# Kernel optimization log

Hardware: AMD Instinct MI355X
Metric: run time of the kernel (lower is better)

The kernel has to match this reference:

```python
import jax, jax.numpy as jnp
import numpy as np

D = 128
POI = 8192
N_HE = 51      # hyperedges (users) in HG_pu
N_UC = 42      # user/category slots at front of UI embedding
LAYERS = 2
TEMP = 0.2


def _l2norm(x):
    n = jnp.linalg.norm(x, axis=-1, keepdims=True)
    return x / jnp.maximum(n, 1e-12)


def _cheby_linear(x, coeffs):
    # x: [N, in], coeffs: [in, out, order+1] -> [N, out]
    x = jnp.tanh(x)
    order = coeffs.shape[-1] - 1
    Ts = [jnp.ones_like(x), x]
    for _ in range(order - 1):
        Ts.append(2.0 * x * Ts[-1] - Ts[-2])
    T = jnp.stack(Ts, axis=-1)  # [N, in, order+1]
    return jnp.einsum('nik,iok->no', T, coeffs)


def _gated_kan(x1, x2, cr, ci):
    # FFT-gated fusion of two [N, D] embeddings (GatedKAN1)
    X1 = jnp.fft.fft(x1, axis=-1)
    X2 = jnp.fft.fft(x2, axis=-1)
    gr = jax.nn.sigmoid(_cheby_linear(X1.real, cr) + _cheby_linear(X2.real, cr))
    fr = gr * X1.real + (1.0 - gr) * X2.real
    gi = jax.nn.sigmoid(_cheby_linear(X1.imag, ci) + _cheby_linear(X2.imag, ci))
    fi = gi * X1.imag + (1.0 - gi) * X2.imag
    return jnp.fft.ifft(fr + 1j * fi, axis=-1).real.astype(x1.dtype)


def _info_nce(z1, z2, temp=TEMP):
    # symmetric InfoNCE with arange labels (diagonal positives)
    z1 = _l2norm(z1)
    z2 = _l2norm(z2)
    sim = jnp.matmul(z1, z2.T) / temp
    l1 = -jnp.mean(jnp.diagonal(jax.nn.log_softmax(sim, axis=1)))
    l2 = -jnp.mean(jnp.diagonal(jax.nn.log_softmax(sim.T, axis=1)))
    return 0.5 * (l1 + l2)


def _hconv(e, HG_pu, HG_up, layers):
    # mean over layer outputs of hypergraph propagation HG_up @ (HG_pu @ e)
    acc = e
    for _ in range(layers):
        e = jnp.matmul(HG_up, jnp.matmul(HG_pu, e))
        acc = acc + e
    return acc / (layers + 1)


def _gconv(e, A, layers):
    acc = e
    for _ in range(layers):
        e = jnp.matmul(A, e)
        acc = acc + e
    return acc / (layers + 1)


def setup_inputs() -> dict:
    key = jax.random.key(0)
    ks = jax.random.split(key, 13)
    inp = {
        'poi_w': jax.random.normal(ks[0], (POI + 1, D), jnp.float32) * 0.02,
        'ui_w': jax.random.normal(ks[1], (POI + 1 + N_UC, D), jnp.float32) * 0.02,
        'w_gate_col': jax.random.normal(ks[2], (D, D), jnp.float32) * 0.08,
        'b_gate_col': jax.random.normal(ks[3], (1, D), jnp.float32) * 0.08,
        'w_gate_U': jax.random.normal(ks[4], (D, D), jnp.float32) * 0.08,
        'b_gate_U': jax.random.normal(ks[5], (1, D), jnp.float32) * 0.08,
        'cheb_real': jax.random.normal(ks[6], (D, D, 4), jnp.float32) / (D * 4),
        'cheb_imag': jax.random.normal(ks[7], (D, D, 4), jnp.float32) / (D * 4),
        'HG_pu': jax.random.uniform(ks[8], (N_HE, POI), jnp.float32) / POI,
        'HG_up': jax.random.uniform(ks[9], (POI, N_HE), jnp.float32) / N_HE,
        'U_I': jax.random.uniform(ks[10], (POI + N_UC, POI + N_UC), jnp.float32) / (POI + N_UC),
        'noise1': jax.random.normal(ks[11], (POI, D), jnp.float32) * 0.1,
        'noise2': jax.random.normal(ks[12], (POI + N_UC, D), jnp.float32) * 0.1,
        'target': 100,
        'user_col': 7,
        'user_ui': 5,
    }
    return inp


def reference(poi_w, ui_w, w_gate_col, b_gate_col, w_gate_U, b_gate_U,
              cheb_real, cheb_imag, HG_pu, HG_up, U_I, noise1, noise2,
              target, user_col, user_ui):
    # gated embedding transforms
    pw = poi_w[:-1]
    col_gate = pw * jax.nn.sigmoid(jnp.matmul(pw, w_gate_col) + b_gate_col)   # [POI, D]
    uw = ui_w[:-1]
    U_gate = uw * jax.nn.sigmoid(jnp.matmul(uw, w_gate_U) + b_gate_U)          # [POI+42, D]

    # hypergraph view
    hg = _l2norm(_hconv(col_gate, HG_pu, HG_up, LAYERS))                        # [POI, D]
    level_loss = _info_nce(hg, hg + noise1)
    hg_users = jnp.matmul(HG_pu, hg)                                            # [51, D]
    hg_user = hg_users[user_col]
    user_cl = hg_users[9:]                                                      # [42, D]

    # user-item graph view
    ue = _l2norm(_gconv(U_gate, U_I, LAYERS))                                   # [POI+42, D]
    level_loss1 = _info_nce(ue, ue + noise2)
    poi_e = ue[N_UC:]                                                           # [POI, D]
    users_emb = ue[user_ui]
    user_c = ue[:N_UC]                                                          # [42, D]

    # FFT-gated Chebyshev-KAN fusion
    final_p = _gated_kan(hg, poi_e, cheb_real, cheb_imag)                       # [POI, D]
    final_u = users_emb + hg_user                                               # [D]
    output = jnp.matmul(final_p, final_u)                                       # [POI]

    pred_loss = -jax.nn.log_softmax(output)[target]
    ssl_p = _info_nce(hg, poi_e)
    ssl = _info_nce(user_c, user_cl)
    loss = pred_loss + (level_loss1 + level_loss) + (ssl_p + ssl)
    return (loss, output)
```

## Files before the change

kernel.cpp:

```cpp
#include <hip/hip_runtime.h>
#include <math.h>

#define D 128
#define P 8192
#define PU 8234
#define NHE 51
#define NUC 42
#define KP 8256

typedef __attribute__((ext_vector_type(8))) short short8v;
typedef __attribute__((ext_vector_type(8))) unsigned short ushort8v;
typedef __attribute__((ext_vector_type(4))) float f32x4;

__device__ inline void atomAddF(float* p, float v) {
#if defined(__HIP_PLATFORM_AMD__)
    unsafeAtomicAdd(p, v);
#else
    atomicAdd(p, v);
#endif
}

__device__ inline unsigned short bfr(float f) {
    unsigned int u = __float_as_uint(f);
    u += 0x7fffu + ((u >> 16) & 1u);
    return (unsigned short)(u >> 16);
}

__global__ void k_tables(float* Cm, float* Sm) {
    int idx = blockIdx.x * 256 + threadIdx.x;
    if (idx >= D * D) return;
    int k = idx >> 7, t = idx & 127;
    int m = (k * t) & 127;
    float ang = (float)m * 0.049087385212340517f;
    Cm[idx] = cosf(ang);
    Sm[idx] = -sinf(ang);
}

__global__ void k_reshape(const float* __restrict__ cr, const float* __restrict__ ci,
                          float* __restrict__ Wr, float* __restrict__ Wi) {
    int idx = blockIdx.x * 256 + threadIdx.x;
    if (idx >= 512 * D) return;
    int o = idx & 127;
    int ik = idx >> 7;
    int i = ik >> 2, kk = ik & 3;
    Wr[idx] = cr[(i * 128 + o) * 4 + kk];
    Wi[idx] = ci[(i * 128 + o) * 4 + kk];
}

#define GEMM_BODY(K_)                                                     \
    {                                                                     \
        float a[4], b[8];                                                 \
        _Pragma("unroll") for (int r = 0; r < 4; r++) a[r] = As[ty + 16 * r][K_]; \
        _Pragma("unroll") for (int c = 0; c < 8; c++) b[c] = Bs[K_][tx + 16 * c]; \
        _Pragma("unroll") for (int r = 0; r < 4; r++)                     \
            _Pragma("unroll") for (int c = 0; c < 8; c++)                 \
                acc[r][c] += a[r] * b[c];                                 \
    }

__global__ __launch_bounds__(256) void k_gemm(const float* __restrict__ A, int lda,
                                              const float* __restrict__ B,
                                              float* __restrict__ C,
                                              int M, int K, float alpha, int klen) {
    __shared__ float As[64][33];
    __shared__ float Bs[32][128];
    const int t = threadIdx.x;
    const int tx = t & 15, ty = t >> 4;
    const int i0 = blockIdx.x * 64;
    const int kbeg = blockIdx.y * klen;
    const int kend = min(K, kbeg + klen);
    float acc[4][8];
#pragma unroll
    for (int r = 0; r < 4; r++)
#pragma unroll
        for (int c = 0; c < 8; c++) acc[r][c] = 0.f;

    for (int k0 = kbeg; k0 < kend; k0 += 32) {
#pragma unroll
        for (int q = 0; q < 2; q++) {
            int idx = t + q * 256;
            int row = idx >> 3;
            int col = (idx & 7) * 4;
            int gi = i0 + row;
#pragma unroll
            for (int u = 0; u < 4; u++) {
                int gk = k0 + col + u;
                As[row][col + u] = (gi < M && gk < kend) ? A[(size_t)gi * lda + gk] : 0.f;
            }
        }
#pragma unroll
        for (int q = 0; q < 4; q++) {
            int idx = t + q * 256;
            int row = idx >> 5;
            int col4 = (idx & 31) * 4;
            int gk = k0 + row;
            float4 v = make_float4(0.f, 0.f, 0.f, 0.f);
            if (gk < kend) v = *reinterpret_cast<const float4*>(B + (size_t)gk * 128 + col4);
            *reinterpret_cast<float4*>(&Bs[row][col4]) = v;
        }
        __syncthreads();
        int klim = min(32, kend - k0);
        if (klim == 32) {
#pragma unroll
            for (int k = 0; k < 32; k++) GEMM_BODY(k)
        } else {
            for (int k = 0; k < klim; k++) GEMM_BODY(k)
        }
        __syncthreads();
    }
#pragma unroll
    for (int r = 0; r < 4; r++) {
        int gi = i0 + ty + 16 * r;
        if (gi < M) {
#pragma unroll
            for (int c = 0; c < 8; c++)
                atomAddF(&C[(size_t)gi * 128 + tx + 16 * c], alpha * acc[r][c]);
        }
    }
}

__global__ void k_small_pu(const float* __restrict__ PUm, const float* __restrict__ X,
                           float* __restrict__ T, int Kn) {
    int i = blockIdx.x;
    int klen = (Kn + gridDim.y - 1) / gridDim.y;
    int kbeg = blockIdx.y * klen;
    int kend = min(Kn, kbeg + klen);
    int t = threadIdx.x;
    int d = t & 127, half = t >> 7;
    float acc = 0.f;
    for (int k = kbeg + half; k < kend; k += 2)
        acc += PUm[(size_t)i * Kn + k] * X[(size_t)k * 128 + d];
    atomAddF(&T[i * 128 + d], acc);
}

__global__ void k_gate_ep(const float* __restrict__ X, const float* __restrict__ pre,
                          const float* __restrict__ bias, float* __restrict__ out, int n) {
    int idx = blockIdx.x * 256 + threadIdx.x;
    if (idx < n) {
        float s = pre[idx] + bias[idx & 127];
        s = 1.f / (1.f + expf(-s));
        out[idx] = X[idx] * s;
    }
}

__global__ void k_acc3norm(const float* __restrict__ a, const float* __restrict__ b,
                           const float* __restrict__ c, float* __restrict__ out) {
    __shared__ float red[128];
    size_t i = blockIdx.x;
    int d = threadIdx.x;
    float v = (a[i * 128 + d] + b[i * 128 + d] + c[i * 128 + d]) * (1.f / 3.f);
    red[d] = v * v;
    __syncthreads();
    for (int s = 64; s > 0; s >>= 1) {
        if (d < s) red[d] += red[d + s];
        __syncthreads();
    }
    float inv = 1.f / fmaxf(sqrtf(red[0]), 1e-12f);
    out[i * 128 + d] = v * inv;
}

__global__ void k_prep(const float* __restrict__ X, const float* __restrict__ Yadd,
                       float scale, unsigned short* __restrict__ Zb) {
    __shared__ float red[128];
    size_t i = blockIdx.x;
    int d = threadIdx.x;
    float v = X[i * 128 + d];
    if (Yadd) v += Yadd[i * 128 + d];
    red[d] = v * v;
    __syncthreads();
    for (int s = 64; s > 0; s >>= 1) {
        if (d < s) red[d] += red[d + s];
        __syncthreads();
    }
    float inv = scale / fmaxf(sqrtf(red[0]), 1e-12f);
    Zb[i * 128 + d] = bfr(v * inv);
}

__global__ __launch_bounds__(256) void k_rowcol_mfma(
    const unsigned short* __restrict__ Za, int n1,
    const unsigned short* __restrict__ Zb, int n2,
    float* __restrict__ rowsum, float* __restrict__ colsum, float* __restrict__ diagsum) {
    __shared__ ushort8v As[2048];
    __shared__ ushort8v Bs[2048];
    const int t = threadIdx.x;
    const int i0 = blockIdx.x * 128, j0 = blockIdx.y * 128;
#pragma unroll
    for (int u = 0; u < 8; ++u) {
        int g = t + u * 256;
        int row = g >> 4, c = g & 15;
        int sw = (row << 4) | (c ^ (row & 15));
        ushort8v va = (ushort8v){0, 0, 0, 0, 0, 0, 0, 0};
        ushort8v vb = va;
        if (i0 + row < n1) va = *(const ushort8v*)(Za + ((size_t)(i0 + row) << 7) + c * 8);
        if (j0 + row < n2) vb = *(const ushort8v*)(Zb + ((size_t)(j0 + row) << 7) + c * 8);
        As[sw] = va;
        Bs[sw] = vb;
    }
    __syncthreads();
    const int l = t & 63, w = t >> 6;
    const int wy = w >> 1, wx = w & 1;
    const int lr = l & 15, lg = l >> 4;
    f32x4 acc[4][4];
#pragma unroll
    for (int mi = 0; mi < 4; ++mi)
#pragma unroll
        for (int ni = 0; ni < 4; ++ni) acc[mi][ni] = (f32x4){0.f, 0.f, 0.f, 0.f};

#pragma unroll
    for (int ks = 0; ks < 4; ++ks) {
        short8v a[4], b[4];
        int c = ks * 4 + lg;
#pragma unroll
        for (int mi = 0; mi < 4; ++mi) {
            int r = wy * 64 + mi * 16 + lr;
            a[mi] = __builtin_bit_cast(short8v, As[(r << 4) | (c ^ (r & 15))]);
            int r2 = wx * 64 + mi * 16 + lr;
            b[mi] = __builtin_bit_cast(short8v, Bs[(r2 << 4) | (c ^ (r2 & 15))]);
        }
#pragma unroll
        for (int mi = 0; mi < 4; ++mi)
#pragma unroll
            for (int ni = 0; ni < 4; ++ni)
                acc[mi][ni] = __builtin_amdgcn_mfma_f32_16x16x32_bf16(a[mi], b[ni], acc[mi][ni], 0, 0, 0);
    }
    float colp[4] = {0.f, 0.f, 0.f, 0.f};
    float dsum = 0.f;
#pragma unroll
    for (int mi = 0; mi < 4; ++mi) {
#pragma unroll
        for (int rg = 0; rg < 4; ++rg) {
            int grow = i0 + wy * 64 + mi * 16 + lg * 4 + rg;
            float rowp = 0.f;
#pragma unroll
            for (int ni = 0; ni < 4; ++ni) {
                int gcol = j0 + wx * 64 + ni * 16 + lr;
                float v = acc[mi][ni][rg];
                bool ok = (grow < n1) && (gcol < n2);
                float e = ok ? __expf(v) : 0.f;
                rowp += e;
                colp[ni] += e;
                if (ok && grow == gcol) dsum += v;
            }
            rowp += __shfl_xor(rowp, 1);
            rowp += __shfl_xor(rowp, 2);
            rowp += __shfl_xor(rowp, 4);
            rowp += __shfl_xor(rowp, 8);
            if (lr == 0 && grow < n1) atomAddF(&rowsum[grow], rowp);
        }
    }
#pragma unroll
    for (int ni = 0; ni < 4; ++ni) {
        float cp = colp[ni];
        cp += __shfl_xor(cp, 16);
        cp += __shfl_xor(cp, 32);
        int gcol = j0 + wx * 64 + ni * 16 + lr;
        if (lg == 0 && gcol < n2) atomAddF(&colsum[gcol], cp);
    }
    if (blockIdx.x == blockIdx.y) {
        dsum += __shfl_xor(dsum, 1);
        dsum += __shfl_xor(dsum, 2);
        dsum += __shfl_xor(dsum, 4);
        dsum += __shfl_xor(dsum, 8);
        dsum += __shfl_xor(dsum, 16);
        dsum += __shfl_xor(dsum, 32);
        if (l == 0) atomAddF(diagsum, dsum);
    }
}

__global__ __launch_bounds__(256) void k_tconv(const float* __restrict__ B,
                                               unsigned short* __restrict__ Bt, int K) {
    __shared__ float tile[32][33];
    int tx = threadIdx.x & 31, ty = threadIdx.x >> 5;
    int k0 = blockIdx.x * 32, c0 = blockIdx.y * 32;
#pragma unroll
    for (int q = 0; q < 4; ++q) {
        int k = k0 + ty + q * 8;
        tile[ty + q * 8][tx] = (k < K) ? B[(size_t)k * 128 + c0 + tx] : 0.f;
    }
    __syncthreads();
#pragma unroll
    for (int q = 0; q < 4; ++q) {
        int c = c0 + ty + q * 8;
        Bt[(size_t)c * KP + k0 + tx] = bfr(tile[tx][ty + q * 8]);
    }
}

__global__ __launch_bounds__(256) void k_gconv(const float* __restrict__ A,
                                               const unsigned short* __restrict__ Bt,
                                               float* __restrict__ C,
                                               int M, int K, int klen) {
    const int t = threadIdx.x;
    const int l = t & 63, w = t >> 6;
    const int lr = l & 15, lg = l >> 4;
    const int r0 = blockIdx.x * 128 + w * 32;
    const int kbeg = blockIdx.y * klen;
    const int kend = min(K, kbeg + klen);
    f32x4 acc[2][8];
#pragma unroll
    for (int mi = 0; mi < 2; ++mi)
#pragma unroll
        for (int ni = 0; ni < 8; ++ni) acc[mi][ni] = (f32x4){0.f, 0.f, 0.f, 0.f};
    size_t rA[2];
    rA[0] = (size_t)min(r0 + lr, M - 1) * (size_t)K;
    rA[1] = (size_t)min(r0 + 16 + lr, M - 1) * (size_t)K;

    for (int k0 = kbeg; k0 < kend; k0 += 32) {
        int kf = k0 + lg * 8;
        short8v a[2];
        if (kf + 8 <= K) {
#pragma unroll
            for (int mi = 0; mi < 2; ++mi) {
                const float* p = A + rA[mi] + kf;
                float2 f0 = *(const float2*)(p);
                float2 f1 = *(const float2*)(p + 2);
                float2 f2 = *(const float2*)(p + 4);
                float2 f3 = *(const float2*)(p + 6);
                short8v v;
                v[0] = (short)bfr(f0.x); v[1] = (short)bfr(f0.y);
                v[2] = (short)bfr(f1.x); v[3] = (short)bfr(f1.y);
                v[4] = (short)bfr(f2.x); v[5] = (short)bfr(f2.y);
                v[6] = (short)bfr(f3.x); v[7] = (short)bfr(f3.y);
                a[mi] = v;
            }
        } else {
#pragma unroll
            for (int mi = 0; mi < 2; ++mi) {
                short8v v;
#pragma unroll
                for (int j = 0; j < 8; ++j) {
                    int kk = kf + j;
                    v[j] = (kk < K) ? (short)bfr(A[rA[mi] + kk]) : (short)0;
                }
                a[mi] = v;
            }
        }
        short8v b[8];
#pragma unroll
        for (int ni = 0; ni < 8; ++ni)
            b[ni] = *(const short8v*)(Bt + (size_t)(ni * 16 + lr) * KP + kf);
#pragma unroll
        for (int mi = 0; mi < 2; ++mi)
#pragma unroll
            for (int ni = 0; ni < 8; ++ni)
                acc[mi][ni] = __builtin_amdgcn_mfma_f32_16x16x32_bf16(a[mi], b[ni], acc[mi][ni], 0, 0, 0);
    }
#pragma unroll
    for (int mi = 0; mi < 2; ++mi) {
#pragma unroll
        for (int rg = 0; rg < 4; ++rg) {
            int gr = r0 + mi * 16 + lg * 4 + rg;
            if (gr < M) {
#pragma unroll
                for (int ni = 0; ni < 8; ++ni)
                    atomAddF(&C[(size_t)gr * 128 + ni * 16 + lr], acc[mi][ni][rg]);
            }
        }
    }
}

__global__ void k_nce_reduce(const float* __restrict__ rs, const float* __restrict__ cs,
                             const float* __restrict__ diag, int n, float* __restrict__ loss) {
    __shared__ float red[256];
    int t = threadIdx.x;
    float s = 0.f;
    for (int i = blockIdx.x * 256 + t; i < n; i += gridDim.x * 256)
        s += logf(rs[i]) + logf(cs[i]);
    red[t] = s;
    __syncthreads();
    for (int st = 128; st > 0; st >>= 1) {
        if (t < st) red[t] += red[t + st];
        __syncthreads();
    }
    if (t == 0) {
        float v = 0.5f * red[0] / (float)n;
        if (blockIdx.x == 0) v -= diag[0] / (float)n;
        atomAddF(loss, v);
    }
}

__global__ void k_ssl(const float* __restrict__ UE, const float* __restrict__ HGU,
                      float* __restrict__ loss) {
    __shared__ float A[NUC][128], B[NUC][128];
    __shared__ float sim[NUC][NUC];
    __shared__ float invA[NUC], invB[NUC];
    __shared__ float pr[64];
    int t = threadIdx.x;
    for (int idx = t; idx < NUC * 128; idx += 256) {
        A[idx >> 7][idx & 127] = UE[idx];
        B[idx >> 7][idx & 127] = HGU[9 * 128 + idx];
    }
    __syncthreads();
    if (t < 2 * NUC) {
        int i = (t < NUC) ? t : t - NUC;
        float s = 0.f;
        if (t < NUC) {
            for (int d = 0; d < 128; d++) { float v = A[i][d]; s += v * v; }
            invA[i] = 1.f / fmaxf(sqrtf(s), 1e-12f);
        } else {
            for (int d = 0; d < 128; d++) { float v = B[i][d]; s += v * v; }
            invB[i] = 1.f / fmaxf(sqrtf(s), 1e-12f);
        }
    }
    __syncthreads();
    for (int idx = t; idx < NUC * NUC; idx += 256) {
        int i = idx / NUC, j = idx % NUC;
        float s = 0.f;
        for (int d = 0; d < 128; d++) s += A[i][d] * B[j][d];
        sim[i][j] = s * invA[i] * invB[j] * 5.0f;
    }
    __syncthreads();
    float part = 0.f;
    if (t < NUC) {
        float rsu = 0.f, csu = 0.f;
        for (int j = 0; j < NUC; j++) {
            rsu += __expf(sim[t][j]);
            csu += __expf(sim[j][t]);
        }
        part = 0.5f * (logf(rsu) + logf(csu)) - sim[t][t];
    }
    if (t < 64) pr[t] = (t < NUC) ? part : 0.f;
    __syncthreads();
    if (t == 0) {
        float s = 0.f;
        for (int i = 0; i < NUC; i++) s += pr[i];
        atomAddF(loss, s / (float)NUC);
    }
}

__global__ void k_features(const float* __restrict__ Xa, const float* __restrict__ Xb,
                           float* __restrict__ G, int n) {
    int idx = blockIdx.x * 256 + threadIdx.x;
    if (idx < n) {
        float x1 = tanhf(Xa[idx]), x2 = tanhf(Xb[idx]);
        float4 w;
        w.x = 2.0f;
        w.y = x1 + x2;
        w.z = (2.f * x1 * x1 - 1.f) + (2.f * x2 * x2 - 1.f);
        w.w = x1 * (4.f * x1 * x1 - 3.f) + x2 * (4.f * x2 * x2 - 3.f);
        *reinterpret_cast<float4*>(G + (size_t)idx * 4) = w;
    }
}

__global__ void k_mix(const float* __restrict__ pre, float* __restrict__ a,
                      const float* __restrict__ b, int n) {
    int idx = blockIdx.x * 256 + threadIdx.x;
    if (idx < n) {
        float g = 1.f / (1.f + expf(-pre[idx]));
        a[idx] = g * a[idx] + (1.f - g) * b[idx];
    }
}

__global__ void k_finalu(const float* __restrict__ UE, const float* __restrict__ HGU,
                         const int* __restrict__ uui, const int* __restrict__ ucol,
                         float* __restrict__ fu) {
    int d = threadIdx.x;
    fu[d] = UE[(size_t)(*uui) * 128 + d] + HGU[(*ucol) * 128 + d];
}

__global__ void k_outvec(const float* __restrict__ FP, const float* __restrict__ fu,
                         float* __restrict__ out) {
    __shared__ float red[128];
    size_t i = blockIdx.x;
    int d = threadIdx.x;
    red[d] = FP[i * 128 + d] * fu[d];
    __syncthreads();
    for (int s = 64; s > 0; s >>= 1) {
        if (d < s) red[d] += red[d + s];
        __syncthreads();
    }
    if (d == 0) out[i] = red[0];
}

__global__ void k_predloss(const float* __restrict__ ov, const int* __restrict__ tgt,
                           float* __restrict__ loss) {
    __shared__ float red[256];
    int t = threadIdx.x;
    float m = -1e30f;
    for (int i = t; i < P; i += 256) m = fmaxf(m, ov[i]);
    red[t] = m;
    __syncthreads();
    for (int s = 128; s > 0; s >>= 1) {
        if (t < s) red[t] = fmaxf(red[t], red[t + s]);
        __syncthreads();
    }
    float mg = red[0];
    __syncthreads();
    float ssum = 0.f;
    for (int i = t; i < P; i += 256) ssum += __expf(ov[i] - mg);
    red[t] = ssum;
    __syncthreads();
    for (int s = 128; s > 0; s >>= 1) {
        if (t < s) red[t] += red[t + s];
        __syncthreads();
    }
    if (t == 0) {
        float lse = mg + logf(red[0]);
        atomAddF(loss, lse - ov[*tgt]);
    }
}

__global__ void k_writeloss(const float* __restrict__ sc, float* __restrict__ out) {
    out[0] = sc[0];
}

extern "C" void kernel_launch(void* const* d_in, const int* in_sizes, int n_in,
                              void* d_out, int out_size, void* d_ws, size_t ws_size,
                              hipStream_t stream) {
    const float* poi_w  = (const float*)d_in[0];
    const float* ui_w   = (const float*)d_in[1];
    const float* Wc     = (const float*)d_in[2];
    const float* bc     = (const float*)d_in[3];
    const float* WU     = (const float*)d_in[4];
    const float* bU     = (const float*)d_in[5];
    const float* cr     = (const float*)d_in[6];
    const float* ci     = (const float*)d_in[7];
    const float* HGpu   = (const float*)d_in[8];
    const float* HGup   = (const float*)d_in[9];
    const float* UI     = (const float*)d_in[10];
    const float* noise1 = (const float*)d_in[11];
    const float* noise2 = (const float*)d_in[12];
    const int* target   = (const int*)d_in[13];
    const int* ucol     = (const int*)d_in[14];
    const int* uui      = (const int*)d_in[15];
    float* out = (float*)d_out;

    float* ws = (float*)d_ws;
    size_t o = 0;
    auto alloc = [&](size_t n) { float* p = ws + o; o += n; return p; };
    float* H   = alloc((size_t)P * D);
    float* UE  = alloc((size_t)PU * D);
    float* B1  = alloc((size_t)PU * D);
    float* B2  = alloc((size_t)PU * D);
    float* B3  = alloc((size_t)PU * D);
    float* B4  = alloc((size_t)PU * D);
    float* G   = alloc((size_t)P * 512);
    float* PRE = alloc((size_t)P * D);
    float* TS  = alloc(NHE * D);
    float* HGU = alloc(NHE * D);
    float* CM  = alloc(D * D);
    float* SM  = alloc(D * D);
    float* WR  = alloc(512 * D);
    float* WI  = alloc(512 * D);
    float* RS  = alloc(8240);
    float* CS  = alloc(8240);
    float* SC  = alloc(16);
    float* FU  = alloc(D);
    unsigned short* ZA = (unsigned short*)alloc((size_t)PU * D / 2);
    unsigned short* ZB = (unsigned short*)alloc((size_t)PU * D / 2);
    unsigned short* ZC = (unsigned short*)alloc((size_t)PU * D / 2);
    unsigned short* BT = (unsigned short*)alloc((size_t)D * KP / 2);
    if (o * sizeof(float) > ws_size) return;

    auto Z = [&](float* p, size_t n) { hipMemsetAsync(p, 0, n * sizeof(float), stream); };
    auto GEMM = [&](const float* A, int lda, const float* B, float* C, int M, int K,
                    int ysplit, float alpha) {
        int klen = (K + ysplit - 1) / ysplit;
        dim3 g((M + 63) / 64, ysplit);
        k_gemm<<<g, 256, 0, stream>>>(A, lda, B, C, M, K, alpha, klen);
    };
    auto GCONV = [&](const float* Xin, float* Cout) {
        k_tconv<<<dim3(KP / 32, 4), 256, 0, stream>>>(Xin, BT, PU);
        int ksplit = 8;
        int klen = ((PU + ksplit - 1) / ksplit + 31) & ~31;
        k_gconv<<<dim3((PU + 127) / 128, ksplit), 256, 0, stream>>>(UI, BT, Cout, PU, PU, klen);
    };
    auto NCE = [&](const unsigned short* z1, int n1, const unsigned short* z2, int n2,
                   float* dslot) {
        Z(RS, n1); Z(CS, n2);
        dim3 g((n1 + 127) / 128, (n2 + 127) / 128);
        k_rowcol_mfma<<<g, 256, 0, stream>>>(z1, n1, z2, n2, RS, CS, dslot);
        k_nce_reduce<<<32, 256, 0, stream>>>(RS, CS, dslot, n1, SC);
    };
    const int EW_P  = (P * D + 255) / 256;
    const int EW_PU = (PU * D + 255) / 256;

    Z(SC, 16);
    k_tables<<<(D * D + 255) / 256, 256, 0, stream>>>(CM, SM);
    k_reshape<<<(512 * D + 255) / 256, 256, 0, stream>>>(cr, ci, WR, WI);

    Z(B2, (size_t)PU * D);
    GEMM(poi_w, D, Wc, B2, P, D, 2, 1.f);
    k_gate_ep<<<EW_P, 256, 0, stream>>>(poi_w, B2, bc, B1, P * D);
    Z(B2, (size_t)PU * D);
    GEMM(ui_w, D, WU, B2, PU, D, 2, 1.f);
    k_gate_ep<<<EW_PU, 256, 0, stream>>>(ui_w, B2, bU, B3, PU * D);

    Z(TS, NHE * D);
    k_small_pu<<<dim3(NHE, 16), 256, 0, stream>>>(HGpu, B1, TS, P);
    Z(B2, (size_t)P * D);
    GEMM(HGup, NHE, TS, B2, P, NHE, 1, 1.f);
    Z(TS, NHE * D);
    k_small_pu<<<dim3(NHE, 16), 256, 0, stream>>>(HGpu, B2, TS, P);
    Z(B4, (size_t)P * D);
    GEMM(HGup, NHE, TS, B4, P, NHE, 1, 1.f);
    k_acc3norm<<<P, 128, 0, stream>>>(B1, B2, B4, H);

    Z(HGU, NHE * D);
    k_small_pu<<<dim3(NHE, 16), 256, 0, stream>>>(HGpu, H, HGU, P);

    k_prep<<<P, 128, 0, stream>>>(H, nullptr, 5.f, ZA);
    k_prep<<<P, 128, 0, stream>>>(H, noise1, 1.f, ZB);
    NCE(ZA, P, ZB, P, SC + 1);

    Z(B2, (size_t)PU * D);
    GCONV(B3, B2);
    Z(B4, (size_t)PU * D);
    GCONV(B2, B4);
    k_acc3norm<<<PU, 128, 0, stream>>>(B3, B2, B4, UE);

    k_prep<<<PU, 128, 0, stream>>>(UE, nullptr, 5.f, ZC);
    k_prep<<<PU, 128, 0, stream>>>(UE, noise2, 1.f, ZB);
    NCE(ZC, PU, ZB, PU, SC + 2);

    const float* poi_e = UE + (size_t)NUC * D;
    k_prep<<<P, 128, 0, stream>>>(poi_e, nullptr, 1.f, ZB);
    NCE(ZA, P, ZB, P, SC + 3);

    k_ssl<<<1, 256, 0, stream>>>(UE, HGU, SC);

    Z(B1, (size_t)P * D); GEMM(H, D, CM, B1, P, D, 2, 1.f);
    Z(B2, (size_t)P * D); GEMM(H, D, SM, B2, P, D, 2, 1.f);
    Z(B3, (size_t)P * D); GEMM(poi_e, D, CM, B3, P, D, 2, 1.f);
    Z(B4, (size_t)P * D); GEMM(poi_e, D, SM, B4, P, D, 2, 1.f);
    k_features<<<EW_P, 256, 0, stream>>>(B1, B3, G, P * D);
    Z(PRE, (size_t)P * D);
    GEMM(G, 512, WR, PRE, P, 512, 4, 1.f);
    k_mix<<<EW_P, 256, 0, stream>>>(PRE, B1, B3, P * D);
    k_features<<<EW_P, 256, 0, stream>>>(B2, B4, G, P * D);
    Z(PRE, (size_t)P * D);
    GEMM(G, 512, WI, PRE, P, 512, 4, 1.f);
    k_mix<<<EW_P, 256, 0, stream>>>(PRE, B2, B4, P * D);
    Z(B3, (size_t)P * D);
    GEMM(B1, D, CM, B3, P, D, 2, 1.f / 128.f);
    GEMM(B2, D, SM, B3, P, D, 2, 1.f / 128.f);

    k_finalu<<<1, 128, 0, stream>>>(UE, HGU, uui, ucol, FU);
    k_outvec<<<P, 128, 0, stream>>>(B3, FU, out + 1);
    k_predloss<<<1, 256, 0, stream>>>(out + 1, target, SC);
    k_writeloss<<<1, 1, 0, stream>>>(SC, out);
}
```

Baseline: 1.519 ms.

## Replace fp32 GEMMs with fused bf16 MFMA kernels for gating, FFT-KAN and output

Replaces the fp32 SIMT GEMM plus separate elementwise kernels with bf16 MFMA GEMMs that fuse their epilogues. These cover the sigmoid gate, the DFT plus Chebyshev feature construction, the gate mix, and the final inverse DFT fused with the dot product against the user vector. It also rewrites the graph convolution kernel to stage A and B tiles in swizzled LDS with a 16-way K split. The aim is to cut memsets, intermediate fp32 round trips and slow FMA GEMMs. In exchange, the DFT and KAN intermediates lose precision by being stored in bf16.

```diff
diff --git a/kernel.cpp b/kernel.cpp
--- a/kernel.cpp
+++ b/kernel.cpp
@@ -10,6 +10,7 @@
 
 typedef __attribute__((ext_vector_type(8))) short short8v;
 typedef __attribute__((ext_vector_type(8))) unsigned short ushort8v;
+typedef __attribute__((ext_vector_type(4))) unsigned short ushort4v;
 typedef __attribute__((ext_vector_type(4))) float f32x4;
 
 __device__ inline void atomAddF(float* p, float v) {
@@ -25,26 +26,318 @@
     u += 0x7fffu + ((u >> 16) & 1u);
     return (unsigned short)(u >> 16);
 }
-
-__global__ void k_tables(float* Cm, float* Sm) {
+__device__ inline float b2f(unsigned short u) {
+    return __uint_as_float(((unsigned int)u) << 16);
+}
+__device__ inline float sigf(float x) { return 1.f / (1.f + __expf(-x)); }
+
+__global__ void k_tables_bf(unsigned short* Ct, unsigned short* St) {
     int idx = blockIdx.x * 256 + threadIdx.x;
     if (idx >= D * D) return;
     int k = idx >> 7, t = idx & 127;
     int m = (k * t) & 127;
     float ang = (float)m * 0.049087385212340517f;
-    Cm[idx] = cosf(ang);
-    Sm[idx] = -sinf(ang);
-}
-
-__global__ void k_reshape(const float* __restrict__ cr, const float* __restrict__ ci,
-                          float* __restrict__ Wr, float* __restrict__ Wi) {
+    Ct[idx] = bfr(cosf(ang));
+    St[idx] = bfr(-sinf(ang));
+}
+
+__global__ void k_reshape_bf(const float* __restrict__ cr, const float* __restrict__ ci,
+                             unsigned short* __restrict__ WRt, unsigned short* __restrict__ WIt) {
     int idx = blockIdx.x * 256 + threadIdx.x;
-    if (idx >= 512 * D) return;
-    int o = idx & 127;
-    int ik = idx >> 7;
+    if (idx >= 128 * 512) return;
+    int o = idx >> 9, ik = idx & 511;
     int i = ik >> 2, kk = ik & 3;
-    Wr[idx] = cr[(i * 128 + o) * 4 + kk];
-    Wi[idx] = ci[(i * 128 + o) * 4 + kk];
+    WRt[idx] = bfr(cr[(i * 128 + o) * 4 + kk]);
+    WIt[idx] = bfr(ci[(i * 128 + o) * 4 + kk]);
+}
+
+__global__ void k_convW(const float* __restrict__ W, unsigned short* __restrict__ Wt) {
+    int idx = blockIdx.x * 256 + threadIdx.x;
+    if (idx >= D * D) return;
+    int n = idx >> 7, k = idx & 127;
+    Wt[idx] = bfr(W[k * 128 + n]);
+}
+
+__device__ inline void mm_stage_B(const unsigned short* __restrict__ Bw, int ldb, int k0,
+                                  unsigned short* Bls, int t) {
+#pragma unroll
+    for (int u = 0; u < 4; ++u) {
+        int idx = u * 256 + t;
+        int row = idx >> 3, c = idx & 7;
+        ushort8v v = *(const ushort8v*)(Bw + (size_t)row * ldb + k0 + c * 8);
+        *(ushort8v*)&Bls[row * 64 + ((c ^ (row & 7)) << 3)] = v;
+    }
+}
+
+__device__ inline void mm_stage_A_f32(const float* __restrict__ A, int lda, int M, int r0,
+                                      int k0, unsigned short* Als, int t) {
+#pragma unroll
+    for (int u = 0; u < 4; ++u) {
+        int idx = u * 256 + t;
+        int row = idx >> 4, c4 = idx & 15;
+        int gr = r0 + row;
+        float4 v = make_float4(0.f, 0.f, 0.f, 0.f);
+        if (gr < M) v = *(const float4*)(A + (size_t)gr * lda + k0 + c4 * 4);
+        ushort4v pv = {bfr(v.x), bfr(v.y), bfr(v.z), bfr(v.w)};
+        *(ushort4v*)&Als[row * 64 + (((c4 >> 1) ^ (row & 7)) << 3) + ((c4 & 1) << 2)] = pv;
+    }
+}
+
+__device__ inline void mm_stage_A_bf(const unsigned short* __restrict__ A, int lda, int M,
+                                     int r0, int k0, unsigned short* Als, int t) {
+#pragma unroll
+    for (int u = 0; u < 2; ++u) {
+        int idx = u * 256 + t;
+        int row = idx >> 3, c = idx & 7;
+        int gr = r0 + row;
+        ushort8v v = (ushort8v){0, 0, 0, 0, 0, 0, 0, 0};
+        if (gr < M) v = *(const ushort8v*)(A + (size_t)gr * lda + k0 + c * 8);
+        *(ushort8v*)&Als[row * 64 + ((c ^ (row & 7)) << 3)] = v;
+    }
+}
+
+__device__ inline void mm_tile_mfma(const unsigned short* Als, const unsigned short* Bls,
+                                    int w, int lr, int lg, f32x4* acc) {
+#pragma unroll
+    for (int s = 0; s < 2; ++s) {
+        int ch = s * 4 + lg;
+        short8v a = *(const short8v*)&Als[(w * 16 + lr) * 64 + ((ch ^ (lr & 7)) << 3)];
+#pragma unroll
+        for (int ni = 0; ni < 8; ++ni) {
+            short8v b = *(const short8v*)&Bls[(ni * 16 + lr) * 64 + ((ch ^ (lr & 7)) << 3)];
+            acc[ni] = __builtin_amdgcn_mfma_f32_16x16x32_bf16(a, b, acc[ni], 0, 0, 0);
+        }
+    }
+}
+
+__global__ __launch_bounds__(256) void k_mm_gate(const float* __restrict__ A,
+                                                 const unsigned short* __restrict__ Wt,
+                                                 const float* __restrict__ bias,
+                                                 float* __restrict__ out, int M) {
+    __shared__ ushort8v AV[512], BV[1024];
+    unsigned short* Als = (unsigned short*)AV;
+    unsigned short* Bls = (unsigned short*)BV;
+    const int t = threadIdx.x, l = t & 63, w = t >> 6, lr = l & 15, lg = l >> 4;
+    const int r0 = blockIdx.x * 64;
+    f32x4 acc[8];
+#pragma unroll
+    for (int ni = 0; ni < 8; ++ni) acc[ni] = (f32x4){0.f, 0.f, 0.f, 0.f};
+    for (int k0 = 0; k0 < 128; k0 += 64) {
+        mm_stage_A_f32(A, 128, M, r0, k0, Als, t);
+        mm_stage_B(Wt, 128, k0, Bls, t);
+        __syncthreads();
+        mm_tile_mfma(Als, Bls, w, lr, lg, acc);
+        __syncthreads();
+    }
+#pragma unroll
+    for (int ni = 0; ni < 8; ++ni) {
+        int col = ni * 16 + lr;
+        float bb = bias[col];
+#pragma unroll
+        for (int rg = 0; rg < 4; ++rg) {
+            int grow = r0 + w * 16 + lg * 4 + rg;
+            if (grow < M) {
+                float x = A[(size_t)grow * 128 + col];
+                out[(size_t)grow * 128 + col] = x * sigf(acc[ni][rg] + bb);
+            }
+        }
+    }
+}
+
+__global__ __launch_bounds__(256) void k_mm_feat(const float* __restrict__ A1,
+                                                 const float* __restrict__ A2,
+                                                 const unsigned short* __restrict__ Wt,
+                                                 unsigned short* __restrict__ G,
+                                                 unsigned short* __restrict__ X1b,
+                                                 unsigned short* __restrict__ X2b, int M) {
+    __shared__ ushort8v AV1[512], AV2[512], BV[1024];
+    unsigned short* Als1 = (unsigned short*)AV1;
+    unsigned short* Als2 = (unsigned short*)AV2;
+    unsigned short* Bls = (unsigned short*)BV;
+    const int t = threadIdx.x, l = t & 63, w = t >> 6, lr = l & 15, lg = l >> 4;
+    const int r0 = blockIdx.x * 64;
+    f32x4 acc1[8], acc2[8];
+#pragma unroll
+    for (int ni = 0; ni < 8; ++ni) {
+        acc1[ni] = (f32x4){0.f, 0.f, 0.f, 0.f};
+        acc2[ni] = (f32x4){0.f, 0.f, 0.f, 0.f};
+    }
+    for (int k0 = 0; k0 < 128; k0 += 64) {
+        mm_stage_A_f32(A1, 128, M, r0, k0, Als1, t);
+        mm_stage_A_f32(A2, 128, M, r0, k0, Als2, t);
+        mm_stage_B(Wt, 128, k0, Bls, t);
+        __syncthreads();
+        mm_tile_mfma(Als1, Bls, w, lr, lg, acc1);
+        mm_tile_mfma(Als2, Bls, w, lr, lg, acc2);
+        __syncthreads();
+    }
+#pragma unroll
+    for (int ni = 0; ni < 8; ++ni) {
+        int col = ni * 16 + lr;
+#pragma unroll
+        for (int rg = 0; rg < 4; ++rg) {
+            int grow = r0 + w * 16 + lg * 4 + rg;
+            if (grow < M) {
+                float v1 = acc1[ni][rg], v2 = acc2[ni][rg];
+                X1b[(size_t)grow * 128 + col] = bfr(v1);
+                X2b[(size_t)grow * 128 + col] = bfr(v2);
+                float x1 = tanhf(v1), x2 = tanhf(v2);
+                ushort4v g4;
+                g4.x = bfr(2.0f);
+                g4.y = bfr(x1 + x2);
+                g4.z = bfr((2.f * x1 * x1 - 1.f) + (2.f * x2 * x2 - 1.f));
+                g4.w = bfr(x1 * (4.f * x1 * x1 - 3.f) + x2 * (4.f * x2 * x2 - 3.f));
+                *(ushort4v*)&G[(size_t)grow * 512 + col * 4] = g4;
+            }
+        }
+    }
+}
+
+__global__ __launch_bounds__(256) void k_mm_mix(const unsigned short* __restrict__ Gb,
+                                                const unsigned short* __restrict__ Wt,
+                                                const unsigned short* __restrict__ X1b,
+                                                const unsigned short* __restrict__ X2b,
+                                                unsigned short* __restrict__ F, int M) {
+    __shared__ ushort8v AV[512], BV[1024];
+    unsigned short* Als = (unsigned short*)AV;
+    unsigned short* Bls = (unsigned short*)BV;
+    const int t = threadIdx.x, l = t & 63, w = t >> 6, lr = l & 15, lg = l >> 4;
+    const int r0 = blockIdx.x * 64;
+    f32x4 acc[8];
+#pragma unroll
+    for (int ni = 0; ni < 8; ++ni) acc[ni] = (f32x4){0.f, 0.f, 0.f, 0.f};
+    for (int k0 = 0; k0 < 512; k0 += 64) {
+        mm_stage_A_bf(Gb, 512, M, r0, k0, Als, t);
+        mm_stage_B(Wt, 512, k0, Bls, t);
+        __syncthreads();
+        mm_tile_mfma(Als, Bls, w, lr, lg, acc);
+        __syncthreads();
+    }
+#pragma unroll
+    for (int ni = 0; ni < 8; ++ni) {
+        int col = ni * 16 + lr;
+#pragma unroll
+        for (int rg = 0; rg < 4; ++rg) {
+            int grow = r0 + w * 16 + lg * 4 + rg;
+            if (grow < M) {
+                float g = sigf(acc[ni][rg]);
+                float x1 = b2f(X1b[(size_t)grow * 128 + col]);
+                float x2 = b2f(X2b[(size_t)grow * 128 + col]);
+                F[(size_t)grow * 128 + col] = bfr(g * x1 + (1.f - g) * x2);
+            }
+        }
+    }
+}
+
+__device__ inline void mm_pair_accum(const unsigned short* A, const unsigned short* Bw, int M,
+                                     int r0, int t, int w, int lr, int lg,
+                                     unsigned short* Als, unsigned short* Bls, f32x4* acc) {
+    for (int k0 = 0; k0 < 128; k0 += 64) {
+        mm_stage_A_bf(A, 128, M, r0, k0, Als, t);
+        mm_stage_B(Bw, 128, k0, Bls, t);
+        __syncthreads();
+        mm_tile_mfma(Als, Bls, w, lr, lg, acc);
+        __syncthreads();
+    }
+}
+
+__global__ __launch_bounds__(256) void k_mm_final(const unsigned short* __restrict__ A0,
+                                                  const unsigned short* __restrict__ B0,
+                                                  const unsigned short* __restrict__ A1,
+                                                  const unsigned short* __restrict__ B1,
+                                                  const float* __restrict__ FU,
+                                                  float* __restrict__ out, int M) {
+    __shared__ ushort8v AV[512], BV[1024];
+    unsigned short* Als = (unsigned short*)AV;
+    unsigned short* Bls = (unsigned short*)BV;
+    const int t = threadIdx.x, l = t & 63, w = t >> 6, lr = l & 15, lg = l >> 4;
+    const int r0 = blockIdx.x * 64;
+    f32x4 acc[8];
+#pragma unroll
+    for (int ni = 0; ni < 8; ++ni) acc[ni] = (f32x4){0.f, 0.f, 0.f, 0.f};
+    mm_pair_accum(A0, B0, M, r0, t, w, lr, lg, Als, Bls, acc);
+    mm_pair_accum(A1, B1, M, r0, t, w, lr, lg, Als, Bls, acc);
+    float fuv[8];
+#pragma unroll
+    for (int ni = 0; ni < 8; ++ni) fuv[ni] = FU[ni * 16 + lr];
+#pragma unroll
+    for (int rg = 0; rg < 4; ++rg) {
+        float v = 0.f;
+#pragma unroll
+        for (int ni = 0; ni < 8; ++ni) v += acc[ni][rg] * fuv[ni];
+        v += __shfl_xor(v, 1);
+        v += __shfl_xor(v, 2);
+        v += __shfl_xor(v, 4);
+        v += __shfl_xor(v, 8);
+        int grow = r0 + w * 16 + lg * 4 + rg;
+        if (lr == 0 && grow < M) out[grow] = v * (1.f / 128.f);
+    }
+}
+
+__global__ __launch_bounds__(256) void k_gconv2(const float* __restrict__ A,
+                                                const unsigned short* __restrict__ Bt,
+                                                float* __restrict__ C,
+                                                int M, int K, int klen) {
+    __shared__ ushort8v AV[1024], BV[1024];
+    unsigned short* Als = (unsigned short*)AV;
+    unsigned short* Bls = (unsigned short*)BV;
+    const int t = threadIdx.x, l = t & 63, w = t >> 6, lr = l & 15, lg = l >> 4;
+    const int r0 = blockIdx.x * 128;
+    const int kbeg = blockIdx.y * klen;
+    const int kend = min(K, kbeg + klen);
+    f32x4 acc[2][8];
+#pragma unroll
+    for (int mi = 0; mi < 2; ++mi)
+#pragma unroll
+        for (int ni = 0; ni < 8; ++ni) acc[mi][ni] = (f32x4){0.f, 0.f, 0.f, 0.f};
+
+    for (int k0 = kbeg; k0 < kend; k0 += 64) {
+#pragma unroll
+        for (int u = 0; u < 16; ++u) {
+            int idx = u * 256 + t;
+            int row = idx >> 5, c2 = idx & 31;
+            int gr = r0 + row, gk = k0 + c2 * 2;
+            float2 v = make_float2(0.f, 0.f);
+            if (gr < M && gk < K) v = *(const float2*)(A + (size_t)gr * K + gk);
+            unsigned int pk = (unsigned int)bfr(v.x) | ((unsigned int)bfr(v.y) << 16);
+            *(unsigned int*)&Als[row * 64 + (((c2 >> 2) ^ (row & 7)) << 3) + ((c2 & 3) << 1)] = pk;
+        }
+#pragma unroll
+        for (int u = 0; u < 4; ++u) {
+            int idx = u * 256 + t;
+            int row = idx >> 3, c = idx & 7;
+            int gk = k0 + c * 8;
+            ushort8v v = (ushort8v){0, 0, 0, 0, 0, 0, 0, 0};
+            if (gk < KP) v = *(const ushort8v*)(Bt + (size_t)row * KP + gk);
+            *(ushort8v*)&Bls[row * 64 + ((c ^ (row & 7)) << 3)] = v;
+        }
+        __syncthreads();
+#pragma unroll
+        for (int s = 0; s < 2; ++s) {
+            int ch = s * 4 + lg;
+            short8v a0 = *(const short8v*)&Als[(w * 32 + lr) * 64 + ((ch ^ (lr & 7)) << 3)];
+            short8v a1 = *(const short8v*)&Als[(w * 32 + 16 + lr) * 64 + ((ch ^ (lr & 7)) << 3)];
+#pragma unroll
+            for (int ni = 0; ni < 8; ++ni) {
+                short8v b = *(const short8v*)&Bls[(ni * 16 + lr) * 64 + ((ch ^ (lr & 7)) << 3)];
+                acc[0][ni] = __builtin_amdgcn_mfma_f32_16x16x32_bf16(a0, b, acc[0][ni], 0, 0, 0);
+                acc[1][ni] = __builtin_amdgcn_mfma_f32_16x16x32_bf16(a1, b, acc[1][ni], 0, 0, 0);
+            }
+        }
+        __syncthreads();
+    }
+#pragma unroll
+    for (int mi = 0; mi < 2; ++mi) {
+#pragma unroll
+        for (int rg = 0; rg < 4; ++rg) {
+            int grow = r0 + w * 32 + mi * 16 + lg * 4 + rg;
+            if (grow < M) {
+#pragma unroll
+                for (int ni = 0; ni < 8; ++ni)
+                    atomAddF(&C[(size_t)grow * 128 + ni * 16 + lr], acc[mi][ni][rg]);
+            }
+        }
+    }
 }
 
 #define GEMM_BODY(K_)                                                     \
@@ -130,16 +423,6 @@
     for (int k = kbeg + half; k < kend; k += 2)
         acc += PUm[(size_t)i * Kn + k] * X[(size_t)k * 128 + d];
     atomAddF(&T[i * 128 + d], acc);
-}
-
-__global__ void k_gate_ep(const float* __restrict__ X, const float* __restrict__ pre,
-                          const float* __restrict__ bias, float* __restrict__ out, int n) {
-    int idx = blockIdx.x * 256 + threadIdx.x;
-    if (idx < n) {
-        float s = pre[idx] + bias[idx & 127];
-        s = 1.f / (1.f + expf(-s));
-        out[idx] = X[idx] * s;
-    }
 }
 
 __global__ void k_acc3norm(const float* __restrict__ a, const float* __restrict__ b,
@@ -284,79 +567,6 @@
     }
 }
 
-__global__ __launch_bounds__(256) void k_gconv(const float* __restrict__ A,
-                                               const unsigned short* __restrict__ Bt,
-                                               float* __restrict__ C,
-                                               int M, int K, int klen) {
-    const int t = threadIdx.x;
-    const int l = t & 63, w = t >> 6;
-    const int lr = l & 15, lg = l >> 4;
-    const int r0 = blockIdx.x * 128 + w * 32;
-    const int kbeg = blockIdx.y * klen;
-    const int kend = min(K, kbeg + klen);
-    f32x4 acc[2][8];
-#pragma unroll
-    for (int mi = 0; mi < 2; ++mi)
-#pragma unroll
-        for (int ni = 0; ni < 8; ++ni) acc[mi][ni] = (f32x4){0.f, 0.f, 0.f, 0.f};
-    size_t rA[2];
-    rA[0] = (size_t)min(r0 + lr, M - 1) * (size_t)K;
-    rA[1] = (size_t)min(r0 + 16 + lr, M - 1) * (size_t)K;
-
-    for (int k0 = kbeg; k0 < kend; k0 += 32) {
-        int kf = k0 + lg * 8;
-        short8v a[2];
-        if (kf + 8 <= K) {
-#pragma unroll
-            for (int mi = 0; mi < 2; ++mi) {
-                const float* p = A + rA[mi] + kf;
-                float2 f0 = *(const float2*)(p);
-                float2 f1 = *(const float2*)(p + 2);
-                float2 f2 = *(const float2*)(p + 4);
-                float2 f3 = *(const float2*)(p + 6);
-                short8v v;
-                v[0] = (short)bfr(f0.x); v[1] = (short)bfr(f0.y);
-                v[2] = (short)bfr(f1.x); v[3] = (short)bfr(f1.y);
-                v[4] = (short)bfr(f2.x); v[5] = (short)bfr(f2.y);
-                v[6] = (short)bfr(f3.x); v[7] = (short)bfr(f3.y);
-                a[mi] = v;
-            }
-        } else {
-#pragma unroll
-            for (int mi = 0; mi < 2; ++mi) {
-                short8v v;
-#pragma unroll
-                for (int j = 0; j < 8; ++j) {
-                    int kk = kf + j;
-                    v[j] = (kk < K) ? (short)bfr(A[rA[mi] + kk]) : (short)0;
-                }
-                a[mi] = v;
-            }
-        }
-        short8v b[8];
-#pragma unroll
-        for (int ni = 0; ni < 8; ++ni)
-            b[ni] = *(const short8v*)(Bt + (size_t)(ni * 16 + lr) * KP + kf);
-#pragma unroll
-        for (int mi = 0; mi < 2; ++mi)
-#pragma unroll
-            for (int ni = 0; ni < 8; ++ni)
-                acc[mi][ni] = __builtin_amdgcn_mfma_f32_16x16x32_bf16(a[mi], b[ni], acc[mi][ni], 0, 0, 0);
-    }
-#pragma unroll
-    for (int mi = 0; mi < 2; ++mi) {
-#pragma unroll
-        for (int rg = 0; rg < 4; ++rg) {
-            int gr = r0 + mi * 16 + lg * 4 + rg;
-            if (gr < M) {
-#pragma unroll
-                for (int ni = 0; ni < 8; ++ni)
-                    atomAddF(&C[(size_t)gr * 128 + ni * 16 + lr], acc[mi][ni][rg]);
-            }
-        }
-    }
-}
-
 __global__ void k_nce_reduce(const float* __restrict__ rs, const float* __restrict__ cs,
                              const float* __restrict__ diag, int n, float* __restrict__ loss) {
     __shared__ float red[256];
@@ -426,48 +636,11 @@
     }
 }
 
-__global__ void k_features(const float* __restrict__ Xa, const float* __restrict__ Xb,
-                           float* __restrict__ G, int n) {
-    int idx = blockIdx.x * 256 + threadIdx.x;
-    if (idx < n) {
-        float x1 = tanhf(Xa[idx]), x2 = tanhf(Xb[idx]);
-        float4 w;
-        w.x = 2.0f;
-        w.y = x1 + x2;
-        w.z = (2.f * x1 * x1 - 1.f) + (2.f * x2 * x2 - 1.f);
-        w.w = x1 * (4.f * x1 * x1 - 3.f) + x2 * (4.f * x2 * x2 - 3.f);
-        *reinterpret_cast<float4*>(G + (size_t)idx * 4) = w;
-    }
-}
-
-__global__ void k_mix(const float* __restrict__ pre, float* __restrict__ a,
-                      const float* __restrict__ b, int n) {
-    int idx = blockIdx.x * 256 + threadIdx.x;
-    if (idx < n) {
-        float g = 1.f / (1.f + expf(-pre[idx]));
-        a[idx] = g * a[idx] + (1.f - g) * b[idx];
-    }
-}
-
 __global__ void k_finalu(const float* __restrict__ UE, const float* __restrict__ HGU,
                          const int* __restrict__ uui, const int* __restrict__ ucol,
                          float* __restrict__ fu) {
     int d = threadIdx.x;
     fu[d] = UE[(size_t)(*uui) * 128 + d] + HGU[(*ucol) * 128 + d];
-}
-
-__global__ void k_outvec(const float* __restrict__ FP, const float* __restrict__ fu,
-                         float* __restrict__ out) {
-    __shared__ float red[128];
-    size_t i = blockIdx.x;
-    int d = threadIdx.x;
-    red[d] = FP[i * 128 + d] * fu[d];
-    __syncthreads();
-    for (int s = 64; s > 0; s >>= 1) {
-        if (d < s) red[d] += red[d + s];
-        __syncthreads();
-    }
-    if (d == 0) out[i] = red[0];
 }
 
 __global__ void k_predloss(const float* __restrict__ ov, const int* __restrict__ tgt,
@@ -525,30 +698,35 @@
 
     float* ws = (float*)d_ws;
     size_t o = 0;
-    auto alloc = [&](size_t n) { float* p = ws + o; o += n; return p; };
+    auto alloc = [&](size_t n) { float* p = ws + o; o += (n + 3) & ~(size_t)3; return p; };
     float* H   = alloc((size_t)P * D);
     float* UE  = alloc((size_t)PU * D);
     float* B1  = alloc((size_t)PU * D);
     float* B2  = alloc((size_t)PU * D);
     float* B3  = alloc((size_t)PU * D);
     float* B4  = alloc((size_t)PU * D);
-    float* G   = alloc((size_t)P * 512);
-    float* PRE = alloc((size_t)P * D);
     float* TS  = alloc(NHE * D);
     float* HGU = alloc(NHE * D);
-    float* CM  = alloc(D * D);
-    float* SM  = alloc(D * D);
-    float* WR  = alloc(512 * D);
-    float* WI  = alloc(512 * D);
     float* RS  = alloc(8240);
     float* CS  = alloc(8240);
     float* SC  = alloc(16);
     float* FU  = alloc(D);
-    unsigned short* ZA = (unsigned short*)alloc((size_t)PU * D / 2);
-    unsigned short* ZB = (unsigned short*)alloc((size_t)PU * D / 2);
-    unsigned short* ZC = (unsigned short*)alloc((size_t)PU * D / 2);
-    unsigned short* BT = (unsigned short*)alloc((size_t)D * KP / 2);
+    unsigned short* ZA  = (unsigned short*)alloc((size_t)PU * D / 2);
+    unsigned short* ZB  = (unsigned short*)alloc((size_t)PU * D / 2);
+    unsigned short* ZC  = (unsigned short*)alloc((size_t)PU * D / 2);
+    unsigned short* BT  = (unsigned short*)alloc((size_t)D * KP / 2);
+    unsigned short* CMt = (unsigned short*)alloc(D * D / 2);
+    unsigned short* SMt = (unsigned short*)alloc(D * D / 2);
+    unsigned short* WRt = (unsigned short*)alloc(D * 512 / 2);
+    unsigned short* WIt = (unsigned short*)alloc(D * 512 / 2);
+    unsigned short* WCt = (unsigned short*)alloc(D * D / 2);
+    unsigned short* WUt = (unsigned short*)alloc(D * D / 2);
+    unsigned short* Gb  = (unsigned short*)alloc((size_t)P * 512 / 2);
     if (o * sizeof(float) > ws_size) return;
+    unsigned short* X1b = ZB;
+    unsigned short* X2b = BT;
+    unsigned short* FRb = ZA;
+    unsigned short* FIb = ZC;
 
     auto Z = [&](float* p, size_t n) { hipMemsetAsync(p, 0, n * sizeof(float), stream); };
     auto GEMM = [&](const float* A, int lda, const float* B, float* C, int M, int K,
@@ -559,9 +737,9 @@
     };
     auto GCONV = [&](const float* Xin, float* Cout) {
         k_tconv<<<dim3(KP / 32, 4), 256, 0, stream>>>(Xin, BT, PU);
-        int ksplit = 8;
-        int klen = ((PU + ksplit - 1) / ksplit + 31) & ~31;
-        k_gconv<<<dim3((PU + 127) / 128, ksplit), 256, 0, stream>>>(UI, BT, Cout, PU, PU, klen);
+        const int ksplit = 16;
+        const int klen = 544;
+        k_gconv2<<<dim3((PU + 127) / 128, ksplit), 256, 0, stream>>>(UI, BT, Cout, PU, PU, klen);
     };
     auto NCE = [&](const unsigned short* z1, int n1, const unsigned short* z2, int n2,
                    float* dslot) {
@@ -570,19 +748,15 @@
         k_rowcol_mfma<<<g, 256, 0, stream>>>(z1, n1, z2, n2, RS, CS, dslot);
         k_nce_reduce<<<32, 256, 0, stream>>>(RS, CS, dslot, n1, SC);
     };
-    const int EW_P  = (P * D + 255) / 256;
-    const int EW_PU = (PU * D + 255) / 256;
 
     Z(SC, 16);
-    k_tables<<<(D * D + 255) / 256, 256, 0, stream>>>(CM, SM);
-    k_reshape<<<(512 * D + 255) / 256, 256, 0, stream>>>(cr, ci, WR, WI);
-
-    Z(B2, (size_t)PU * D);
-    GEMM(poi_w, D, Wc, B2, P, D, 2, 1.f);
-    k_gate_ep<<<EW_P, 256, 0, stream>>>(poi_w, B2, bc, B1, P * D);
-    Z(B2, (size_t)PU * D);
-    GEMM(ui_w, D, WU, B2, PU, D, 2, 1.f);
-    k_gate_ep<<<EW_PU, 256, 0, stream>>>(ui_w, B2, bU, B3, PU * D);
+    k_tables_bf<<<64, 256, 0, stream>>>(CMt, SMt);
+    k_reshape_bf<<<256, 256, 0, stream>>>(cr, ci, WRt, WIt);
+    k_convW<<<64, 256, 0, stream>>>(Wc, WCt);
+    k_convW<<<64, 256, 0, stream>>>(WU, WUt);
+
+    k_mm_gate<<<(P + 63) / 64, 256, 0, stream>>>(poi_w, WCt, bc, B1, P);
+    k_mm_gate<<<(PU + 63) / 64, 256, 0, stream>>>(ui_w, WUt, bU, B3, PU);
 
     Z(TS, NHE * D);
     k_small_pu<<<dim3(NHE, 16), 256, 0, stream>>>(HGpu, B1, TS, P);
@@ -617,24 +791,13 @@
 
     k_ssl<<<1, 256, 0, stream>>>(UE, HGU, SC);
 
-    Z(B1, (size_t)P * D); GEMM(H, D, CM, B1, P, D, 2, 1.f);
-    Z(B2, (size_t)P * D); GEMM(H, D, SM, B2, P, D, 2, 1.f);
-    Z(B3, (size_t)P * D); GEMM(poi_e, D, CM, B3, P, D, 2, 1.f);
-    Z(B4, (size_t)P * D); GEMM(poi_e, D, SM, B4, P, D, 2, 1.f);
-    k_features<<<EW_P, 256, 0, stream>>>(B1, B3, G, P * D);
-    Z(PRE, (size_t)P * D);
-    GEMM(G, 512, WR, PRE, P, 512, 4, 1.f);
-    k_mix<<<EW_P, 256, 0, stream>>>(PRE, B1, B3, P * D);
-    k_features<<<EW_P, 256, 0, stream>>>(B2, B4, G, P * D);
-    Z(PRE, (size_t)P * D);
-    GEMM(G, 512, WI, PRE, P, 512, 4, 1.f);
-    k_mix<<<EW_P, 256, 0, stream>>>(PRE, B2, B4, P * D);
-    Z(B3, (size_t)P * D);
-    GEMM(B1, D, CM, B3, P, D, 2, 1.f / 128.f);
-    GEMM(B2, D, SM, B3, P, D, 2, 1.f / 128.f);
+    k_mm_feat<<<P / 64, 256, 0, stream>>>(H, poi_e, CMt, Gb, X1b, X2b, P);
+    k_mm_mix<<<P / 64, 256, 0, stream>>>(Gb, WRt, X1b, X2b, FRb, P);
+    k_mm_feat<<<P / 64, 256, 0, stream>>>(H, poi_e, SMt, Gb, X1b, X2b, P);
+    k_mm_mix<<<P / 64, 256, 0, stream>>>(Gb, WIt, X1b, X2b, FIb, P);
 
     k_finalu<<<1, 128, 0, stream>>>(UE, HGU, uui, ucol, FU);
-    k_outvec<<<P, 128, 0, stream>>>(B3, FU, out + 1);
+    k_mm_final<<<P / 64, 256, 0, stream>>>(FRb, CMt, FIb, SMt, FU, out + 1, P);
     k_predloss<<<1, 256, 0, stream>>>(out + 1, target, SC);
     k_writeloss<<<1, 1, 0, stream>>>(SC, out);
 }
```

Measured after the change: 1.442 ms. 5.0% less time.
